# Kernel tuning notes

Measured on AMD Instinct MI355X. Metric: run time of the kernel, lower is better.

Reference implementation:

```python
import jax, jax.numpy as jnp
import numpy as np

K = 2  # num_experts_per_token


def setup_inputs() -> dict:
    key = jax.random.key(0)
    ks = jax.random.split(key, 5)
    B, T, D, E, H = 2, 2048, 768, 8, 1536
    x = jax.random.normal(ks[0], (B, T, D), dtype=jnp.float32)
    gate_w = jax.random.normal(ks[1], (E, D), dtype=jnp.float32) * (1.0 / np.sqrt(D))
    gate_bank = jax.random.normal(ks[2], (E, D, H), dtype=jnp.float32) * (1.0 / np.sqrt(D))
    up_bank = jax.random.normal(ks[3], (E, D, H), dtype=jnp.float32) * (1.0 / np.sqrt(D))
    down_bank = jax.random.normal(ks[4], (E, H, D), dtype=jnp.float32) * (1.0 / np.sqrt(H))
    return {"x": x, "gate_w": gate_w, "gate_bank": gate_bank,
            "up_bank": up_bank, "down_bank": down_bank}


def reference(x, gate_w, gate_bank, up_bank, down_bank):
    # x: [B,T,D]; gate_w: [E,D]; banks: [E,D,H]/[E,D,H]/[E,H,D]
    # Eval mode: no gate noise (module only adds noise when training).
    logits = jnp.einsum('btd,ed->bte', x, gate_w)                  # [B,T,E]
    probs = jax.nn.softmax(logits, axis=-1)
    selected_probs, selected_idx = jax.lax.top_k(probs, K)          # [B,T,K]
    selected_probs = selected_probs / (
        jnp.sum(selected_probs, axis=-1, keepdims=True) + 1e-8)

    a = jnp.einsum('btd,edh->bteh', x, gate_bank)                   # [B,T,E,H]
    u = jnp.einsum('btd,edh->bteh', x, up_bank)
    h = jax.nn.silu(a) * u
    y_all = jnp.einsum('bteh,ehd->bted', h, down_bank)              # [B,T,E,D]

    # Gather the top-k experts' outputs and combine with normalized weights.
    y_sel = jnp.take_along_axis(y_all, selected_idx[..., None], axis=2)  # [B,T,K,D]
    y = jnp.sum(y_sel * selected_probs[..., None], axis=2)          # [B,T,D]
    return y
```

## Files before the change

### kernel.cpp

```cpp
#include <hip/hip_runtime.h>
#include <hip/hip_bf16.h>

#define NTOK 4096
#define DDIM 768
#define EEXP 8
#define HDIM 1536
#define MBLK 128
#define MAXMB 72
#define CAP  (MAXMB * MBLK)
#define NENT (NTOK * 2)
#define RTHREADS 1024
#define EPT (NENT / RTHREADS)

typedef float f32x4 __attribute__((ext_vector_type(4)));
typedef __bf16 bf16x8 __attribute__((ext_vector_type(8)));
typedef __bf16 bf16x4 __attribute__((ext_vector_type(4)));

static const size_t XB_OFF   = 0;
static const size_t GT_OFF   = 6291456;
static const size_t UT_OFF   = GT_OFF + 18874368;
static const size_t YB_OFF   = GT_OFF;
static const size_t DT_OFF   = UT_OFF + 18874368;
static const size_t HB_OFF   = DT_OFF + 18874368;
static const size_t TKI_OFF  = HB_OFF + 28311552;
static const size_t TKW_OFF  = TKI_OFF + NENT*4;
static const size_t PT_OFF   = TKW_OFF + NENT*4;
static const size_t SL_OFF   = PT_OFF + CAP*4;
static const size_t CTRL_OFF = SL_OFF + NENT*4;
static const size_t WS_NEEDED = CTRL_OFF + 1024;

#define GLOAD16(g, l) __builtin_amdgcn_global_load_lds( \
    (const __attribute__((address_space(1))) void*)(g),  \
    (__attribute__((address_space(3))) void*)(l), 16, 0, 0)

#define MFMA_BF16 __builtin_amdgcn_mfma_f32_16x16x32_bf16



__global__ __launch_bounds__(256) void convert_x_kernel(
    const float* __restrict__ x, __bf16* __restrict__ xb, int n4)
{
    int i = blockIdx.x * 256 + threadIdx.x;
    if (i < n4) {
        f32x4 v = reinterpret_cast<const f32x4*>(x)[i];
        bf16x4 o;
        o[0] = (__bf16)v[0]; o[1] = (__bf16)v[1];
        o[2] = (__bf16)v[2]; o[3] = (__bf16)v[3];
        reinterpret_cast<bf16x4*>(xb)[i] = o;
    }
}

__global__ __launch_bounds__(256) void transpose_all_kernel(
    const float* __restrict__ gb, const float* __restrict__ ub,
    const float* __restrict__ db, __bf16* __restrict__ Gt,
    __bf16* __restrict__ Ut, __bf16* __restrict__ Dt)
{
    __shared__ float tile[64][65];
    int z = blockIdx.z, bank = z >> 3, e = z & 7;
    int R, C, r0, c0;
    const float* s;
    __bf16* d;
    if (bank < 2) {
        R = DDIM; C = HDIM;
        s = (bank == 0 ? gb : ub) + (size_t)e * DDIM * HDIM;
        d = (bank == 0 ? Gt : Ut) + (size_t)e * DDIM * HDIM;
        c0 = blockIdx.x * 64; r0 = blockIdx.y * 64;
    } else {
        R = HDIM; C = DDIM;
        s = db + (size_t)e * DDIM * HDIM;
        d = Dt + (size_t)e * DDIM * HDIM;
        r0 = blockIdx.x * 64; c0 = blockIdx.y * 64;
    }
    int tx = threadIdx.x & 15, ty = threadIdx.x >> 4;
#pragma unroll
    for (int j = 0; j < 4; j++) {
        int r = ty + j * 16;
        f32x4 v = *reinterpret_cast<const f32x4*>(&s[(size_t)(r0 + r) * C + c0 + tx * 4]);
        tile[r][tx*4+0] = v[0]; tile[r][tx*4+1] = v[1];
        tile[r][tx*4+2] = v[2]; tile[r][tx*4+3] = v[3];
    }
    __syncthreads();
#pragma unroll
    for (int j = 0; j < 4; j++) {
        int c = ty + j * 16;
        bf16x4 o;
#pragma unroll
        for (int i = 0; i < 4; i++) o[i] = (__bf16)tile[tx*4+i][c];
        *reinterpret_cast<bf16x4*>(&d[(size_t)(c0 + c) * R + r0 + tx*4]) = o;
    }
}

__global__ __launch_bounds__(256) void gating_kernel(
    const float* __restrict__ x, const float* __restrict__ gw,
    int* __restrict__ topk_idx, float* __restrict__ topk_w)
{
    int lane = threadIdx.x & 63;
    int t = blockIdx.x * 4 + (threadIdx.x >> 6);
    const float* xr = x + (size_t)t * DDIM;
    float acc[EEXP];
#pragma unroll
    for (int e = 0; e < EEXP; e++) acc[e] = 0.0f;
    for (int i = 0; i < DDIM / 64; i++) {
        int d = lane + i * 64;
        float xv = xr[d];
#pragma unroll
        for (int e = 0; e < EEXP; e++) acc[e] += xv * gw[e * DDIM + d];
    }
#pragma unroll
    for (int e = 0; e < EEXP; e++) {
        for (int off = 32; off; off >>= 1) acc[e] += __shfl_xor(acc[e], off);
    }
    if (lane == 0) {
        float m = acc[0];
#pragma unroll
        for (int e = 1; e < EEXP; e++) m = fmaxf(m, acc[e]);
        float p[EEXP], sum = 0.0f;
#pragma unroll
        for (int e = 0; e < EEXP; e++) { p[e] = expf(acc[e] - m); sum += p[e]; }
        int i0 = 0; float b0 = acc[0];
#pragma unroll
        for (int e = 1; e < EEXP; e++) if (acc[e] > b0) { b0 = acc[e]; i0 = e; }
        int i1 = -1; float b1 = -3.4e38f;
#pragma unroll
        for (int e = 0; e < EEXP; e++) if (e != i0 && acc[e] > b1) { b1 = acc[e]; i1 = e; }
        float pr0 = p[i0] / sum, pr1 = p[i1] / sum;
        float den = pr0 + pr1 + 1e-8f;
        topk_idx[2*t]   = i0; topk_w[2*t]   = pr0 / den;
        topk_idx[2*t+1] = i1; topk_w[2*t+1] = pr1 / den;
    }
}

__global__ __launch_bounds__(RTHREADS) void route_kernel(
    const int* __restrict__ topk_idx, int* __restrict__ ctrl,
    int* __restrict__ pair_token, int* __restrict__ slot_of)
{
    __shared__ int wt[EEXP][16];
    __shared__ int wpre[EEXP][16];
    __shared__ int base[EEXP];

    int tid = threadIdx.x;
    int lane = tid & 63, wv = tid >> 6;

    for (int i = tid; i < CAP; i += RTHREADS) pair_token[i] = 0;

    int e_of[EPT];
    int c[EEXP];
#pragma unroll
    for (int e = 0; e < EEXP; e++) c[e] = 0;
#pragma unroll
    for (int j = 0; j < EPT; j++) {
        int e = topk_idx[tid * EPT + j];
        e_of[j] = e;
        c[e]++;
    }

    int pre[EEXP];
#pragma unroll
    for (int e = 0; e < EEXP; e++) {
        int v = c[e];
        for (int d = 1; d < 64; d <<= 1) {
            int u = __shfl_up(v, d);
            if (lane >= d) v += u;
        }
        pre[e] = v - c[e];
        if (lane == 63) wt[e][wv] = v;
    }
    __syncthreads();

    if (tid == 0) {
        int off = 0, gmb = 0;
        for (int e = 0; e < EEXP; e++) {
            int run = 0;
            for (int w = 0; w < 16; w++) { wpre[e][w] = run; run += wt[e][w]; }
            base[e] = off;
            int nmb = (run + MBLK - 1) >> 7;
            for (int i = 0; i < nmb; i++) ctrl[32 + gmb++] = e;
            off += nmb << 7;
        }
        ctrl[24] = gmb;
    }
    __syncthreads();

    int run[EEXP];
#pragma unroll
    for (int e = 0; e < EEXP; e++) run[e] = base[e] + wpre[e][wv] + pre[e];
#pragma unroll
    for (int j = 0; j < EPT; j++) {
        int ent = tid * EPT + j;
        int e = e_of[j];
        int slot = run[e]++;
        pair_token[slot] = ent >> 1;
        slot_of[ent] = slot;
    }
}

__global__ __launch_bounds__(256, 2) void gateup_kernel(
    const __bf16* __restrict__ xb, const __bf16* __restrict__ Gt,
    const __bf16* __restrict__ Ut, const int* __restrict__ ctrl,
    const int* __restrict__ pair_token, __bf16* __restrict__ hbuf)
{
    int bid = blockIdx.x;
    int swz = (bid & 7) * (MAXMB * 12 / 8) + (bid >> 3);
    int mb = swz / 12, y = swz - mb * 12;
    if (mb >= ctrl[24]) return;
    int e = ctrl[32 + mb];
    int hbase = y * 128;
    const __bf16* G = Gt + (size_t)e * HDIM * DDIM;
    const __bf16* U = Ut + (size_t)e * HDIM * DDIM;

    __shared__ __bf16 lds[3 * 8192];

    int tid = threadIdx.x;
    int lane = tid & 63, w = tid >> 6;
    int wr = w >> 1, wc = w & 1;

    int lr = tid >> 3;
    int lc = ((tid & 7) ^ (lr & 7)) << 3;
    const __bf16* gA[4];
#pragma unroll
    for (int j = 0; j < 4; j++) {
        int tok = pair_token[mb * MBLK + j * 32 + lr];
        gA[j] = xb + (size_t)tok * DDIM + lc;
    }
    const __bf16* gG = G + (size_t)(hbase + lr) * DDIM + lc;
    const __bf16* gU = U + (size_t)(hbase + lr) * DDIM + lc;
    const size_t rstep = (size_t)32 * DDIM;

    f32x4 accg[4][4], accu[4][4];
#pragma unroll
    for (int m = 0; m < 4; m++)
#pragma unroll
        for (int n = 0; n < 4; n++) { accg[m][n] = (f32x4)0.0f; accu[m][n] = (f32x4)0.0f; }

    for (int kk = 0; kk < DDIM; kk += 64) {
#pragma unroll
        for (int j = 0; j < 4; j++)
            GLOAD16(gA[j] + kk, &lds[j * 2048 + tid * 8]);
#pragma unroll
        for (int j = 0; j < 4; j++)
            GLOAD16(gG + kk + j * rstep, &lds[8192 + j * 2048 + tid * 8]);
#pragma unroll
        for (int j = 0; j < 4; j++)
            GLOAD16(gU + kk + j * rstep, &lds[16384 + j * 2048 + tid * 8]);
        __syncthreads();

#pragma unroll
        for (int ks = 0; ks < 2; ks++) {
            int kb = ks * 32 + (lane >> 4) * 8;
            bf16x8 af[4], bg[4], bu[4];
#pragma unroll
            for (int m = 0; m < 4; m++) {
                int row = wr * 64 + m * 16 + (lane & 15);
                af[m] = *reinterpret_cast<const bf16x8*>(
                    &lds[row * 64 + (kb ^ ((row & 7) << 3))]);
            }
#pragma unroll
            for (int n = 0; n < 4; n++) {
                int col = wc * 64 + n * 16 + (lane & 15);
                int ba = col * 64 + (kb ^ ((col & 7) << 3));
                bg[n] = *reinterpret_cast<const bf16x8*>(&lds[8192 + ba]);
                bu[n] = *reinterpret_cast<const bf16x8*>(&lds[16384 + ba]);
            }
#pragma unroll
            for (int n = 0; n < 4; n++)
#pragma unroll
                for (int m = 0; m < 4; m++) {
                    accg[m][n] = MFMA_BF16(af[m], bg[n], accg[m][n], 0, 0, 0);
                    accu[m][n] = MFMA_BF16(af[m], bu[n], accu[m][n], 0, 0, 0);
                }
        }
        __syncthreads();
    }

    size_t slotbase = (size_t)mb * MBLK;
#pragma unroll
    for (int m = 0; m < 4; m++)
#pragma unroll
        for (int n = 0; n < 4; n++)
#pragma unroll
            for (int r = 0; r < 4; r++) {
                int row = wr * 64 + m * 16 + (lane >> 4) * 4 + r;
                int col = hbase + wc * 64 + n * 16 + (lane & 15);
                float a = accg[m][n][r], u = accu[m][n][r];
                float hv = (a / (1.0f + expf(-a))) * u;
                hbuf[(slotbase + row) * HDIM + col] = (__bf16)hv;
            }
}

__global__ __launch_bounds__(256, 3) void down_kernel(
    const __bf16* __restrict__ hbuf, const __bf16* __restrict__ Dt,
    const int* __restrict__ ctrl, float* __restrict__ ybuf)
{
    int bid = blockIdx.x;
    int swz = (bid & 7) * (MAXMB * 6 / 8) + (bid >> 3);
    int mb = swz / 6, y = swz - mb * 6;
    if (mb >= ctrl[24]) return;
    int e = ctrl[32 + mb];
    int dbase = y * 128;
    const __bf16* Dn = Dt + (size_t)e * DDIM * HDIM;

    __shared__ __bf16 lds[2 * 8192];

    int tid = threadIdx.x;
    int lane = tid & 63, w = tid >> 6;
    int wr = w >> 1, wc = w & 1;

    int lr = tid >> 3;
    int lc = ((tid & 7) ^ (lr & 7)) << 3;
    const __bf16* gA = hbuf + (size_t)(mb * MBLK + lr) * HDIM + lc;
    const __bf16* gB = Dn + (size_t)(dbase + lr) * HDIM + lc;
    const size_t rstep = (size_t)32 * HDIM;

    f32x4 acc[4][4];
#pragma unroll
    for (int m = 0; m < 4; m++)
#pragma unroll
        for (int n = 0; n < 4; n++) acc[m][n] = (f32x4)0.0f;

    for (int kk = 0; kk < HDIM; kk += 64) {
#pragma unroll
        for (int j = 0; j < 4; j++)
            GLOAD16(gA + kk + j * rstep, &lds[j * 2048 + tid * 8]);
#pragma unroll
        for (int j = 0; j < 4; j++)
            GLOAD16(gB + kk + j * rstep, &lds[8192 + j * 2048 + tid * 8]);
        __syncthreads();

#pragma unroll
        for (int ks = 0; ks < 2; ks++) {
            int kb = ks * 32 + (lane >> 4) * 8;
            bf16x8 af[4], bd[4];
#pragma unroll
            for (int m = 0; m < 4; m++) {
                int row = wr * 64 + m * 16 + (lane & 15);
                af[m] = *reinterpret_cast<const bf16x8*>(
                    &lds[row * 64 + (kb ^ ((row & 7) << 3))]);
            }
#pragma unroll
            for (int n = 0; n < 4; n++) {
                int col = wc * 64 + n * 16 + (lane & 15);
                bd[n] = *reinterpret_cast<const bf16x8*>(
                    &lds[8192 + col * 64 + (kb ^ ((col & 7) << 3))]);
            }
#pragma unroll
            for (int n = 0; n < 4; n++)
#pragma unroll
                for (int m = 0; m < 4; m++)
                    acc[m][n] = MFMA_BF16(af[m], bd[n], acc[m][n], 0, 0, 0);
        }
        __syncthreads();
    }

#pragma unroll
    for (int m = 0; m < 4; m++)
#pragma unroll
        for (int n = 0; n < 4; n++)
#pragma unroll
            for (int r = 0; r < 4; r++) {
                int row = wr * 64 + m * 16 + (lane >> 4) * 4 + r;
                int col = dbase + wc * 64 + n * 16 + (lane & 15);
                ybuf[(size_t)(mb * MBLK + row) * DDIM + col] = acc[m][n][r];
            }
}

__global__ __launch_bounds__(192) void combine_kernel(
    const float* __restrict__ ybuf, const int* __restrict__ slot_of,
    const float* __restrict__ topk_w, float* __restrict__ out)
{
    int t = blockIdx.x;
    int q = threadIdx.x;
    int s0 = slot_of[2*t], s1 = slot_of[2*t+1];
    float w0 = topk_w[2*t], w1 = topk_w[2*t+1];
    f32x4 y0 = reinterpret_cast<const f32x4*>(ybuf + (size_t)s0 * DDIM)[q];
    f32x4 y1 = reinterpret_cast<const f32x4*>(ybuf + (size_t)s1 * DDIM)[q];
    f32x4 o;
#pragma unroll
    for (int r = 0; r < 4; r++) o[r] = w0 * y0[r] + w1 * y1[r];
    reinterpret_cast<f32x4*>(out + (size_t)t * DDIM)[q] = o;
}

extern "C" void kernel_launch(void* const* d_in, const int* in_sizes, int n_in,
                              void* d_out, int out_size, void* d_ws, size_t ws_size,
                              hipStream_t stream)
{
    if (ws_size < WS_NEEDED) return;

    const float* x      = (const float*)d_in[0];
    const float* gate_w = (const float*)d_in[1];
    const float* gbank  = (const float*)d_in[2];
    const float* ubank  = (const float*)d_in[3];
    const float* dbank  = (const float*)d_in[4];
    float* out = (float*)d_out;

    char* ws = (char*)d_ws;
    __bf16* xb   = (__bf16*)(ws + XB_OFF);
    __bf16* Gt   = (__bf16*)(ws + GT_OFF);
    __bf16* Ut   = (__bf16*)(ws + UT_OFF);
    float*  ybuf = (float*)(ws + YB_OFF);
    __bf16* Dt   = (__bf16*)(ws + DT_OFF);
    __bf16* hbuf = (__bf16*)(ws + HB_OFF);
    int*    tki  = (int*)(ws + TKI_OFF);
    float*  tkw  = (float*)(ws + TKW_OFF);
    int*    pt   = (int*)(ws + PT_OFF);
    int*    slot = (int*)(ws + SL_OFF);
    int*    ctrl = (int*)(ws + CTRL_OFF);

    convert_x_kernel<<<(NTOK * DDIM / 4 + 255) / 256, 256, 0, stream>>>(x, xb, NTOK * DDIM / 4);
    transpose_all_kernel<<<dim3(24, 12, 24), 256, 0, stream>>>(gbank, ubank, dbank, Gt, Ut, Dt);

    gating_kernel<<<NTOK / 4, 256, 0, stream>>>(x, gate_w, tki, tkw);
    route_kernel<<<1, RTHREADS, 0, stream>>>(tki, ctrl, pt, slot);

    gateup_kernel<<<MAXMB * (HDIM / 128), 256, 0, stream>>>(xb, Gt, Ut, ctrl, pt, hbuf);
    down_kernel<<<MAXMB * (DDIM / 128), 256, 0, stream>>>(hbuf, Dt, ctrl, ybuf);
    combine_kernel<<<NTOK, 192, 0, stream>>>(ybuf, slot, tkw, out);
}
```

Before: 140.6 us.

## Fuse x conversion into gating and merge routing with weight transpose kernel

The bf16 conversion of x moves into the gating kernel, removing a separate launch and a second read of x. Routing and the weight transposes now share one 1024-thread launch: block 0 does routing while the other blocks each transpose a 64x64 tile. The K loops of the gate/up and down GEMMs are also fully unrolled. Together these cut kernel launches and let the single-block routing step overlap the transpose work, at the cost of larger code and more register pressure from the unrolling.

```diff
diff --git a/kernel.cpp b/kernel.cpp
--- a/kernel.cpp
+++ b/kernel.cpp
@@ -11,6 +11,7 @@
 #define NENT (NTOK * 2)
 #define RTHREADS 1024
 #define EPT (NENT / RTHREADS)
+#define NTTILE 6912
 
 typedef float f32x4 __attribute__((ext_vector_type(4)));
 typedef __bf16 bf16x8 __attribute__((ext_vector_type(8)));
@@ -36,27 +37,120 @@
 #define MFMA_BF16 __builtin_amdgcn_mfma_f32_16x16x32_bf16
 
 
-
-__global__ __launch_bounds__(256) void convert_x_kernel(
-    const float* __restrict__ x, __bf16* __restrict__ xb, int n4)
-{
-    int i = blockIdx.x * 256 + threadIdx.x;
-    if (i < n4) {
-        f32x4 v = reinterpret_cast<const f32x4*>(x)[i];
-        bf16x4 o;
-        o[0] = (__bf16)v[0]; o[1] = (__bf16)v[1];
-        o[2] = (__bf16)v[2]; o[3] = (__bf16)v[3];
-        reinterpret_cast<bf16x4*>(xb)[i] = o;
-    }
-}
-
-__global__ __launch_bounds__(256) void transpose_all_kernel(
+__global__ __launch_bounds__(256) void gating_kernel(
+    const float* __restrict__ x, const float* __restrict__ gw,
+    int* __restrict__ topk_idx, float* __restrict__ topk_w,
+    __bf16* __restrict__ xb)
+{
+    int lane = threadIdx.x & 63;
+    int t = blockIdx.x * 4 + (threadIdx.x >> 6);
+    const float* xr = x + (size_t)t * DDIM;
+    __bf16* xbr = xb + (size_t)t * DDIM;
+    float acc[EEXP];
+#pragma unroll
+    for (int e = 0; e < EEXP; e++) acc[e] = 0.0f;
+#pragma unroll
+    for (int i = 0; i < DDIM / 64; i++) {
+        int d = lane + i * 64;
+        float xv = xr[d];
+        xbr[d] = (__bf16)xv;
+#pragma unroll
+        for (int e = 0; e < EEXP; e++) acc[e] += xv * gw[e * DDIM + d];
+    }
+#pragma unroll
+    for (int e = 0; e < EEXP; e++) {
+        for (int off = 32; off; off >>= 1) acc[e] += __shfl_xor(acc[e], off);
+    }
+    if (lane == 0) {
+        float m = acc[0];
+#pragma unroll
+        for (int e = 1; e < EEXP; e++) m = fmaxf(m, acc[e]);
+        float p[EEXP], sum = 0.0f;
+#pragma unroll
+        for (int e = 0; e < EEXP; e++) { p[e] = expf(acc[e] - m); sum += p[e]; }
+        int i0 = 0; float b0 = acc[0];
+#pragma unroll
+        for (int e = 1; e < EEXP; e++) if (acc[e] > b0) { b0 = acc[e]; i0 = e; }
+        int i1 = -1; float b1 = -3.4e38f;
+#pragma unroll
+        for (int e = 0; e < EEXP; e++) if (e != i0 && acc[e] > b1) { b1 = acc[e]; i1 = e; }
+        float pr0 = p[i0] / sum, pr1 = p[i1] / sum;
+        float den = pr0 + pr1 + 1e-8f;
+        topk_idx[2*t]   = i0; topk_w[2*t]   = pr0 / den;
+        topk_idx[2*t+1] = i1; topk_w[2*t+1] = pr1 / den;
+    }
+}
+
+__global__ __launch_bounds__(RTHREADS) void mega_kernel(
     const float* __restrict__ gb, const float* __restrict__ ub,
     const float* __restrict__ db, __bf16* __restrict__ Gt,
-    __bf16* __restrict__ Ut, __bf16* __restrict__ Dt)
+    __bf16* __restrict__ Ut, __bf16* __restrict__ Dt,
+    const int* __restrict__ topk_idx, int* __restrict__ ctrl,
+    int* __restrict__ pair_token, int* __restrict__ slot_of)
 {
     __shared__ float tile[64][65];
-    int z = blockIdx.z, bank = z >> 3, e = z & 7;
+    __shared__ int wt[EEXP][16];
+    __shared__ int wpre[EEXP][16];
+    __shared__ int base[EEXP];
+
+    int tid = threadIdx.x;
+
+    if (blockIdx.x == 0) {
+        int lane = tid & 63, wv = tid >> 6;
+        for (int i = tid; i < CAP; i += RTHREADS) pair_token[i] = 0;
+
+        int e_of[EPT];
+        int c[EEXP];
+#pragma unroll
+        for (int e = 0; e < EEXP; e++) c[e] = 0;
+#pragma unroll
+        for (int j = 0; j < EPT; j++) {
+            int e = topk_idx[tid * EPT + j];
+            e_of[j] = e;
+            c[e]++;
+        }
+        int pre[EEXP];
+#pragma unroll
+        for (int e = 0; e < EEXP; e++) {
+            int v = c[e];
+            for (int d = 1; d < 64; d <<= 1) {
+                int u = __shfl_up(v, d);
+                if (lane >= d) v += u;
+            }
+            pre[e] = v - c[e];
+            if (lane == 63) wt[e][wv] = v;
+        }
+        __syncthreads();
+        if (tid == 0) {
+            int off = 0, gmb = 0;
+            for (int e = 0; e < EEXP; e++) {
+                int run = 0;
+                for (int w = 0; w < 16; w++) { wpre[e][w] = run; run += wt[e][w]; }
+                base[e] = off;
+                int nmb = (run + MBLK - 1) >> 7;
+                for (int i = 0; i < nmb; i++) ctrl[32 + gmb++] = e;
+                off += nmb << 7;
+            }
+            ctrl[24] = gmb;
+        }
+        __syncthreads();
+        int run[EEXP];
+#pragma unroll
+        for (int e = 0; e < EEXP; e++) run[e] = base[e] + wpre[e][wv] + pre[e];
+#pragma unroll
+        for (int j = 0; j < EPT; j++) {
+            int ent = tid * EPT + j;
+            int e = e_of[j];
+            int slot = run[e]++;
+            pair_token[slot] = ent >> 1;
+            slot_of[ent] = slot;
+        }
+        return;
+    }
+
+    int bt = blockIdx.x - 1;
+    int z = bt / 288, rem = bt - z * 288;
+    int bank = z >> 3, e = z & 7;
     int R, C, r0, c0;
     const float* s;
     __bf16* d;
@@ -64,133 +158,25 @@
         R = DDIM; C = HDIM;
         s = (bank == 0 ? gb : ub) + (size_t)e * DDIM * HDIM;
         d = (bank == 0 ? Gt : Ut) + (size_t)e * DDIM * HDIM;
-        c0 = blockIdx.x * 64; r0 = blockIdx.y * 64;
+        c0 = (rem % 24) * 64; r0 = (rem / 24) * 64;
     } else {
         R = HDIM; C = DDIM;
         s = db + (size_t)e * DDIM * HDIM;
         d = Dt + (size_t)e * DDIM * HDIM;
-        r0 = blockIdx.x * 64; c0 = blockIdx.y * 64;
-    }
-    int tx = threadIdx.x & 15, ty = threadIdx.x >> 4;
-#pragma unroll
-    for (int j = 0; j < 4; j++) {
-        int r = ty + j * 16;
-        f32x4 v = *reinterpret_cast<const f32x4*>(&s[(size_t)(r0 + r) * C + c0 + tx * 4]);
-        tile[r][tx*4+0] = v[0]; tile[r][tx*4+1] = v[1];
-        tile[r][tx*4+2] = v[2]; tile[r][tx*4+3] = v[3];
+        r0 = (rem % 24) * 64; c0 = (rem / 24) * 64;
+    }
+    int tx = tid & 15, ty = tid >> 4;
+    {
+        f32x4 v = *reinterpret_cast<const f32x4*>(&s[(size_t)(r0 + ty) * C + c0 + tx * 4]);
+        tile[ty][tx*4+0] = v[0]; tile[ty][tx*4+1] = v[1];
+        tile[ty][tx*4+2] = v[2]; tile[ty][tx*4+3] = v[3];
     }
     __syncthreads();
-#pragma unroll
-    for (int j = 0; j < 4; j++) {
-        int c = ty + j * 16;
+    {
         bf16x4 o;
 #pragma unroll
-        for (int i = 0; i < 4; i++) o[i] = (__bf16)tile[tx*4+i][c];
-        *reinterpret_cast<bf16x4*>(&d[(size_t)(c0 + c) * R + r0 + tx*4]) = o;
-    }
-}
-
-__global__ __launch_bounds__(256) void gating_kernel(
-    const float* __restrict__ x, const float* __restrict__ gw,
-    int* __restrict__ topk_idx, float* __restrict__ topk_w)
-{
-    int lane = threadIdx.x & 63;
-    int t = blockIdx.x * 4 + (threadIdx.x >> 6);
-    const float* xr = x + (size_t)t * DDIM;
-    float acc[EEXP];
-#pragma unroll
-    for (int e = 0; e < EEXP; e++) acc[e] = 0.0f;
-    for (int i = 0; i < DDIM / 64; i++) {
-        int d = lane + i * 64;
-        float xv = xr[d];
-#pragma unroll
-        for (int e = 0; e < EEXP; e++) acc[e] += xv * gw[e * DDIM + d];
-    }
-#pragma unroll
-    for (int e = 0; e < EEXP; e++) {
-        for (int off = 32; off; off >>= 1) acc[e] += __shfl_xor(acc[e], off);
-    }
-    if (lane == 0) {
-        float m = acc[0];
-#pragma unroll
-        for (int e = 1; e < EEXP; e++) m = fmaxf(m, acc[e]);
-        float p[EEXP], sum = 0.0f;
-#pragma unroll
-        for (int e = 0; e < EEXP; e++) { p[e] = expf(acc[e] - m); sum += p[e]; }
-        int i0 = 0; float b0 = acc[0];
-#pragma unroll
-        for (int e = 1; e < EEXP; e++) if (acc[e] > b0) { b0 = acc[e]; i0 = e; }
-        int i1 = -1; float b1 = -3.4e38f;
-#pragma unroll
-        for (int e = 0; e < EEXP; e++) if (e != i0 && acc[e] > b1) { b1 = acc[e]; i1 = e; }
-        float pr0 = p[i0] / sum, pr1 = p[i1] / sum;
-        float den = pr0 + pr1 + 1e-8f;
-        topk_idx[2*t]   = i0; topk_w[2*t]   = pr0 / den;
-        topk_idx[2*t+1] = i1; topk_w[2*t+1] = pr1 / den;
-    }
-}
-
-__global__ __launch_bounds__(RTHREADS) void route_kernel(
-    const int* __restrict__ topk_idx, int* __restrict__ ctrl,
-    int* __restrict__ pair_token, int* __restrict__ slot_of)
-{
-    __shared__ int wt[EEXP][16];
-    __shared__ int wpre[EEXP][16];
-    __shared__ int base[EEXP];
-
-    int tid = threadIdx.x;
-    int lane = tid & 63, wv = tid >> 6;
-
-    for (int i = tid; i < CAP; i += RTHREADS) pair_token[i] = 0;
-
-    int e_of[EPT];
-    int c[EEXP];
-#pragma unroll
-    for (int e = 0; e < EEXP; e++) c[e] = 0;
-#pragma unroll
-    for (int j = 0; j < EPT; j++) {
-        int e = topk_idx[tid * EPT + j];
-        e_of[j] = e;
-        c[e]++;
-    }
-
-    int pre[EEXP];
-#pragma unroll
-    for (int e = 0; e < EEXP; e++) {
-        int v = c[e];
-        for (int d = 1; d < 64; d <<= 1) {
-            int u = __shfl_up(v, d);
-            if (lane >= d) v += u;
-        }
-        pre[e] = v - c[e];
-        if (lane == 63) wt[e][wv] = v;
-    }
-    __syncthreads();
-
-    if (tid == 0) {
-        int off = 0, gmb = 0;
-        for (int e = 0; e < EEXP; e++) {
-            int run = 0;
-            for (int w = 0; w < 16; w++) { wpre[e][w] = run; run += wt[e][w]; }
-            base[e] = off;
-            int nmb = (run + MBLK - 1) >> 7;
-            for (int i = 0; i < nmb; i++) ctrl[32 + gmb++] = e;
-            off += nmb << 7;
-        }
-        ctrl[24] = gmb;
-    }
-    __syncthreads();
-
-    int run[EEXP];
-#pragma unroll
-    for (int e = 0; e < EEXP; e++) run[e] = base[e] + wpre[e][wv] + pre[e];
-#pragma unroll
-    for (int j = 0; j < EPT; j++) {
-        int ent = tid * EPT + j;
-        int e = e_of[j];
-        int slot = run[e]++;
-        pair_token[slot] = ent >> 1;
-        slot_of[ent] = slot;
+        for (int i = 0; i < 4; i++) o[i] = (__bf16)tile[tx*4+i][ty];
+        *reinterpret_cast<bf16x4*>(&d[(size_t)(c0 + ty) * R + r0 + tx*4]) = o;
     }
 }
 
@@ -232,7 +218,9 @@
 #pragma unroll
         for (int n = 0; n < 4; n++) { accg[m][n] = (f32x4)0.0f; accu[m][n] = (f32x4)0.0f; }
 
-    for (int kk = 0; kk < DDIM; kk += 64) {
+#pragma unroll
+    for (int kt = 0; kt < DDIM / 64; kt++) {
+        const int kk = kt * 64;
 #pragma unroll
         for (int j = 0; j < 4; j++)
             GLOAD16(gA[j] + kk, &lds[j * 2048 + tid * 8]);
@@ -317,7 +305,9 @@
 #pragma unroll
         for (int n = 0; n < 4; n++) acc[m][n] = (f32x4)0.0f;
 
-    for (int kk = 0; kk < HDIM; kk += 64) {
+#pragma unroll
+    for (int kt = 0; kt < HDIM / 64; kt++) {
+        const int kk = kt * 64;
 #pragma unroll
         for (int j = 0; j < 4; j++)
             GLOAD16(gA + kk + j * rstep, &lds[j * 2048 + tid * 8]);
@@ -405,11 +395,9 @@
     int*    slot = (int*)(ws + SL_OFF);
     int*    ctrl = (int*)(ws + CTRL_OFF);
 
-    convert_x_kernel<<<(NTOK * DDIM / 4 + 255) / 256, 256, 0, stream>>>(x, xb, NTOK * DDIM / 4);
-    transpose_all_kernel<<<dim3(24, 12, 24), 256, 0, stream>>>(gbank, ubank, dbank, Gt, Ut, Dt);
-
-    gating_kernel<<<NTOK / 4, 256, 0, stream>>>(x, gate_w, tki, tkw);
-    route_kernel<<<1, RTHREADS, 0, stream>>>(tki, ctrl, pt, slot);
+    gating_kernel<<<NTOK / 4, 256, 0, stream>>>(x, gate_w, tki, tkw, xb);
+    mega_kernel<<<NTTILE + 1, RTHREADS, 0, stream>>>(
+        gbank, ubank, dbank, Gt, Ut, Dt, tki, ctrl, pt, slot);
 
     gateup_kernel<<<MAXMB * (HDIM / 128), 256, 0, stream>>>(xb, Gt, Ut, ctrl, pt, hbuf);
     down_kernel<<<MAXMB * (DDIM / 128), 256, 0, stream>>>(hbuf, Dt, ctrl, ybuf);
```

Result: faster. 125.4 us (-10.8%).
